# Kernel tuning notes

Hardware: AMD Instinct MI355X
Metric: run time of the kernel (lower is better)

The kernel has to match this reference:

```python
import jax, jax.numpy as jnp
import numpy as np

N = 2048      # num graph nodes (activities + places)
D = 256       # embedding_size
C = 3 * D     # cat_embedding_size
V = 2         # num variants
L = 16        # activities per variant
E = 16 * N    # edges for the encoder GNN
DEG_P = 0.0156  # adjacency density (~32 out-degree)


def setup_inputs() -> dict:
    key = jax.random.key(0)
    ks = jax.random.split(key, 6)
    embeddings = jax.random.normal(ks[0], (N, D), dtype=jnp.float32)
    W_self = jax.random.normal(ks[1], (D, D), dtype=jnp.float32) * 0.05
    W_nbr = jax.random.normal(ks[2], (D, D), dtype=jnp.float32) * 0.05
    b = jnp.zeros((D,), dtype=jnp.float32)
    variants = jax.random.randint(ks[3], (V, L), 0, N, dtype=jnp.int32)
    original = (jax.random.uniform(ks[4], (N, N)) < DEG_P).astype(jnp.int32)
    edge_index = jax.random.randint(ks[5], (2, E), 0, N, dtype=jnp.int32)
    return {"embeddings": embeddings, "W_self": W_self, "W_nbr": W_nbr, "b": b,
            "variants": variants, "original": original, "edge_index": edge_index}


def _forward(embeddings, W_self, W_nbr, b, variants, original, edge_index):
    n, d = embeddings.shape
    c = 3 * d
    dt = embeddings.dtype
    adj = original.astype(dt)              # [N,N]; adj[i,j]=1 iff edge i->j (forward star = row)
    src_e, dst_e = edge_index[0], edge_index[1]

    def encoder(x):
        # SecondEncoder approximated as one GCN-style message-passing layer
        msg = jax.ops.segment_sum(x[src_e], dst_e, num_segments=n)
        return jax.nn.relu(x @ W_self + msg @ W_nbr + b)

    def run_variant(acts):  # acts: [L] int32
        onehot = jax.nn.one_hot(acts, n, dtype=dt)                # [L,N]
        incl = jnp.flip(jnp.cumsum(jnp.flip(onehot, 0), 0), 0)    # sum_{j>=i} onehot[j]
        present_later = ((incl - onehot) > 0).astype(dt)          # set of nodes in acts[i+1:]

        def step(carry, inp):
            emb, pi, summary = carry
            a, plater = inp
            followers = adj[a]                                    # forward star of activity a
            has = jnp.any(followers > 0)
            adj_m = adj * plater[None, :]                         # edges into later-in-variant activities
            dest_cnt = adj_m.sum(axis=1)                          # |destination set| per candidate place
            dst_all = adj_m @ emb                                 # summed destination embeddings, [N,D]
            mask = jnp.where(has, ((followers > 0) & (dest_cnt > 0)).astype(dt), 0.0)
            # cat = (place_f, src_f, dst_f) per considered place
            cat = jnp.concatenate(
                [emb, jnp.broadcast_to(emb[a][None, :], emb.shape), dst_all], axis=1) * mask[:, None]
            pi = pi + cat                                         # places_info[place] += cat
            # prev_embedding_summary += places_info[place] for each considered place
            summary = summary + (mask[:, None] * pi).sum(axis=0)
            # places_info[considered] += prev_embedding_summary
            pi = pi + mask[:, None] * summary[None, :]
            emb = jnp.where(has, encoder(emb), emb)               # encoder skipped when no followers
            return (emb, pi, summary), None

        init = (embeddings, jnp.zeros((n, c), dt), jnp.zeros((c,), dt))
        (_, pi, _), _ = jax.lax.scan(step, init, (acts, present_later))
        return pi

    # variant shuffle in the original is irrelevant: embeddings reset each variant
    # and final_places_info is a sum over variants.
    return jax.vmap(run_variant)(variants).sum(axis=0)


def reference(embeddings, W_self, W_nbr, b, variants, original, edge_index):
    return _forward(embeddings, W_self, W_nbr, b, variants, original, edge_index)
```

## Files before the change

### kernel.cpp

```cpp
#include <hip/hip_runtime.h>

#define N 2048
#define D 256
#define C 768
#define V 2
#define L 16
#define NSTATE 15
#define NAPP 14
#define TCAP 256
#define FCAP 64

typedef __attribute__((ext_vector_type(8))) short bf16x8;
typedef __attribute__((ext_vector_type(4))) float f32x4;

__device__ __forceinline__ ushort bf16_rn(float x) {
  unsigned u = __float_as_uint(x);
  u += 0x7FFFu + ((u >> 16) & 1u);
  return (ushort)(u >> 16);
}
__device__ __forceinline__ float bf16_f(ushort h) {
  return __uint_as_float(((unsigned)h) << 16);
}

__device__ __forceinline__ size_t a_addr(int row, int k) {
  return ((size_t)(row >> 5) * 4 + (k >> 6)) * 2048 + (row & 31) * 64 + (k & 63);
}
__device__ __forceinline__ size_t wt_addr(int n, int k) {
  return ((size_t)(n >> 5) * 4 + (k >> 6)) * 2048 + (n & 31) * 64 + (k & 63);
}

__global__ __launch_bounds__(256) void k_init(
    const float* __restrict__ emb, const float* __restrict__ Ws,
    const float* __restrict__ Wn, float* __restrict__ states0,
    ushort* __restrict__ WtHi, ushort* __restrict__ WtLo,
    ushort* __restrict__ A0hi, ushort* __restrict__ A0lo,
    float* __restrict__ out,
    const int* __restrict__ adj, const int* __restrict__ variants,
    int* __restrict__ stepP, int* __restrict__ stepDm,
    int* __restrict__ stepCnt, int* __restrict__ hasG, int* __restrict__ tlG) {
  __shared__ int tl_sh[16];
  __shared__ int foll[FCAP], fbits[FCAP];
  __shared__ int sh_tc, sh_fcnt, sh_ecnt;
  int t = threadIdx.x;
  if (blockIdx.x < 512) {
    size_t i = (size_t)blockIdx.x * 256 + t;
    const size_t stride = (size_t)512 * 256;
    for (size_t x = i; x < (size_t)N * D; x += stride) {
      float v = emb[x];
      states0[x] = v;
      ushort h = bf16_rn(v);
      ushort l = bf16_rn(v - bf16_f(h));
      size_t a = a_addr((int)(x >> 8), (int)(x & 255));
      A0hi[a] = h;
      A0lo[a] = l;
    }
    for (size_t x = i; x < (size_t)512 * 256; x += stride) {
      int n = (int)(x >> 8), k = (int)(x & 255);
      float v = (n < 256) ? Ws[(size_t)k * 256 + n]
                          : Wn[(size_t)k * 256 + (n - 256)];
      ushort h = bf16_rn(v);
      size_t a = wt_addr(n, k);
      WtHi[a] = h;
      WtLo[a] = bf16_rn(v - bf16_f(h));
    }
    for (size_t x = i; x < (size_t)N * C; x += stride) out[x] = 0.f;
    return;
  }
  int vi = blockIdx.x - 512;
  int v = vi / L, i = vi % L;
  int a = variants[vi];
  if (t == 0) {
    int cnt = 0;
    for (int j = i + 1; j < L; j++) {
      int x = variants[v * L + j];
      bool dup = false;
      for (int q = 0; q < cnt; q++) if (tl_sh[q] == x) dup = true;
      if (!dup) tl_sh[cnt++] = x;
    }
    sh_tc = cnt;
    sh_fcnt = 0;
    sh_ecnt = 0;
    for (int q = 0; q < cnt; q++) tlG[vi * 16 + q] = tl_sh[q];
  }
  __syncthreads();
  for (int p = t; p < N; p += 256) {
    if (adj[(size_t)a * N + p] != 0) {
      int f = atomicAdd(&sh_fcnt, 1);
      if (f < FCAP) foll[f] = p;
    }
  }
  __syncthreads();
  int fc = sh_fcnt < FCAP ? sh_fcnt : FCAP;
  int tc = sh_tc;
  for (int x = t; x < fc; x += 256) fbits[x] = 0;
  __syncthreads();
  for (int x = t; x < fc * tc; x += 256) {
    int fi = x / tc, q = x - fi * tc;
    if (adj[(size_t)foll[fi] * N + tl_sh[q]] != 0) atomicOr(&fbits[fi], 1 << q);
  }
  __syncthreads();
  for (int fi = t; fi < fc; fi += 256) {
    int bits = fbits[fi];
    if (bits) {
      int e = atomicAdd(&sh_ecnt, 1);
      stepP[vi * FCAP + e] = foll[fi];
      stepDm[vi * FCAP + e] = bits;
    }
  }
  __syncthreads();
  if (t == 0) {
    stepCnt[vi] = sh_ecnt;
    hasG[vi] = (sh_fcnt > 0);
  }
}

__global__ __launch_bounds__(1024) void k_scan(const int* __restrict__ ei,
                                               int E, int* __restrict__ fillpos,
                                               int* __restrict__ row_ptr) {
  __shared__ int hist[N];
  __shared__ int part[256];
  __shared__ int base[257];
  int t = threadIdx.x;
  for (int p = t; p < N; p += 1024) hist[p] = 0;
  __syncthreads();
  const int e4 = E >> 2;
  const int4* dsts = (const int4*)(ei + E);
  for (int g = t; g < e4; g += 1024) {
    int4 d = dsts[g];
    atomicAdd(&hist[d.x], 1);
    atomicAdd(&hist[d.y], 1);
    atomicAdd(&hist[d.z], 1);
    atomicAdd(&hist[d.w], 1);
  }
  for (int e = (e4 << 2) + t; e < E; e += 1024) atomicAdd(&hist[ei[E + e]], 1);
  __syncthreads();
  int v[8];
  int s = 0;
  if (t < 256) {
    for (int j = 0; j < 8; j++) { v[j] = hist[t * 8 + j]; s += v[j]; }
  }
  __syncthreads();
  if (t < 256) part[t] = s;
  __syncthreads();
  if (t == 0) {
    int acc = 0;
    for (int q = 0; q < 256; q++) { base[q] = acc; acc += part[q]; }
    base[256] = acc;
  }
  __syncthreads();
  if (t < 256) {
    int acc = base[t];
    for (int j = 0; j < 8; j++) {
      row_ptr[t * 8 + j] = acc;
      fillpos[t * 8 + j] = acc;
      acc += v[j];
    }
    if (t == 255) row_ptr[N] = base[256];
  }
}

__global__ __launch_bounds__(256) void k_fillB(
    const int* __restrict__ ei, int E, int* __restrict__ fillpos,
    int* __restrict__ csr_src,
    const int* __restrict__ stepP, const int* __restrict__ stepDm,
    const int* __restrict__ stepCnt, const int* __restrict__ hasG,
    int* __restrict__ entP, int* __restrict__ entPrev, int* __restrict__ entDm,
    int* __restrict__ offsG, int* __restrict__ kidxG, int* __restrict__ cmatG,
    int* __restrict__ lastPG, int* __restrict__ lastIG, int* __restrict__ lastMG,
    int* __restrict__ cntG) {
  __shared__ int pmask[N];
  __shared__ int sP[16][FCAP];
  __shared__ int sDm[16][FCAP];
  __shared__ int cnt[16], offs[17];
  __shared__ int cmat_sh[256];
  __shared__ int sh_u;
  int t = threadIdx.x;
  if (blockIdx.x < 128) {
    for (int e = blockIdx.x * 256 + t; e < E; e += 128 * 256) {
      int dst = ei[E + e];
      int pos = atomicAdd(&fillpos[dst], 1);
      csr_src[pos] = ei[e];
    }
    return;
  }
  int v = blockIdx.x - 128;
  for (int p = t; p < N; p += 256) pmask[p] = 0;
  for (int x = t; x < 256; x += 256) cmat_sh[x] = 0;
  if (t < 16) cnt[t] = stepCnt[v * L + t];
  if (t == 0) sh_u = 0;
  __syncthreads();
  if (t == 0) {
    int acc = 0;
    for (int i = 0; i < 16; i++) {
      offs[i] = acc < TCAP ? acc : TCAP;
      acc += cnt[i];
    }
    offs[16] = acc < TCAP ? acc : TCAP;
    cntG[v * 2 + 0] = offs[16];
    int k = 0;
    for (int i = 0; i < L; i++) {
      kidxG[v * 16 + i] = k;
      if (hasG[v * L + i]) k++;
    }
  }
  for (int x = t; x < 16 * FCAP; x += 256) {
    int i = x >> 6, f = x & 63;
    if (f < stepCnt[v * L + i]) {
      int p = stepP[(v * L + i) * FCAP + f];
      sP[i][f] = p;
      sDm[i][f] = stepDm[(v * L + i) * FCAP + f];
      atomicOr(&pmask[p], 1 << i);
    }
  }
  __syncthreads();
  for (int x = t; x < 16 * FCAP; x += 256) {
    int i = x >> 6, f = x & 63;
    if (f < cnt[i]) {
      int e = offs[i] + f;
      if (e < TCAP) {
        int p = sP[i][f];
        entP[v * TCAP + e] = p;
        entDm[v * TCAP + e] = sDm[i][f];
        int m = pmask[p] & ((1 << i) - 1);
        int prev = -1;
        if (m) {
          int j = 31 - __clz(m);
          int cj = cnt[j];
          for (int f2 = 0; f2 < cj; f2++)
            if (sP[j][f2] == p) { prev = offs[j] + f2; break; }
        }
        entPrev[v * TCAP + e] = prev;
      }
    }
  }
  __syncthreads();
  for (int p = t; p < N; p += 256) {
    int m = pmask[p];
    if (m) {
      int u = atomicAdd(&sh_u, 1);
      int j = 31 - __clz(m);
      int li = -1;
      int cj = cnt[j];
      for (int f2 = 0; f2 < cj; f2++)
        if (sP[j][f2] == p) { li = offs[j] + f2; break; }
      lastPG[v * TCAP + u] = p;
      lastIG[v * TCAP + u] = li;
      lastMG[v * TCAP + u] = m;
      int mm = m;
      while (mm) {
        int bi = __ffs(mm) - 1; mm &= mm - 1;
        int m2 = m & ((1 << bi) - 1);
        while (m2) {
          int bj = __ffs(m2) - 1; m2 &= m2 - 1;
          atomicAdd(&cmat_sh[bi * 16 + bj], 1);
        }
      }
    }
  }
  __syncthreads();
  if (t == 0) cntG[v * 2 + 1] = sh_u;
  for (int x = t; x < 256; x += 256) cmatG[v * 256 + x] = cmat_sh[x];
  for (int x = t; x < 17; x += 256) offsG[v * 17 + x] = offs[x];
}

__global__ __launch_bounds__(256) void k_gemm(
    const ushort* __restrict__ Ah, const ushort* __restrict__ Al,
    const ushort* __restrict__ Wh_g, const ushort* __restrict__ Wl_g,
    float* __restrict__ Z) {
  __shared__ __align__(16) ushort Ash[2][32][72], Asl[2][32][72];
  __shared__ __align__(16) ushort Wsh[2][32][72], Wsl[2][32][72];
  const int tid = threadIdx.x, wave = tid >> 6, lane = tid & 63;
  const int quad = lane >> 4, l16 = lane & 15;
  const int wr = wave >> 1, wc = wave & 1;
  const int mb = blockIdx.x, nb = blockIdx.y;
  const int sr = tid >> 3, sc = (tid & 7) * 8;

  f32x4 acc = {0.f, 0.f, 0.f, 0.f};
  size_t abase = (size_t)mb * 4 * 2048 + (size_t)tid * 8;
  size_t wbase = (size_t)nb * 4 * 2048 + (size_t)tid * 8;
  {
    uint4 ra  = *(const uint4*)&Ah[abase];
    uint4 rl  = *(const uint4*)&Al[abase];
    uint4 rwh = *(const uint4*)&Wh_g[wbase];
    uint4 rwl = *(const uint4*)&Wl_g[wbase];
    *(uint4*)&Ash[0][sr][sc] = ra;
    *(uint4*)&Asl[0][sr][sc] = rl;
    *(uint4*)&Wsh[0][sr][sc] = rwh;
    *(uint4*)&Wsl[0][sr][sc] = rwl;
  }
  __syncthreads();
#pragma unroll
  for (int c = 0; c < 4; c++) {
    const int rb = c & 1;
    uint4 ra, rl, rwh, rwl;
    if (c < 3) {
      size_t o = (size_t)(c + 1) * 2048;
      ra  = *(const uint4*)&Ah[abase + o];
      rl  = *(const uint4*)&Al[abase + o];
      rwh = *(const uint4*)&Wh_g[wbase + o];
      rwl = *(const uint4*)&Wl_g[wbase + o];
    }
#pragma unroll
    for (int kf = 0; kf < 2; kf++) {
      int ko = kf * 32 + quad * 8;
      bf16x8 a_h = *(const bf16x8*)&Ash[rb][wr * 16 + l16][ko];
      bf16x8 a_l = *(const bf16x8*)&Asl[rb][wr * 16 + l16][ko];
      bf16x8 w_h = *(const bf16x8*)&Wsh[rb][wc * 16 + l16][ko];
      bf16x8 w_l = *(const bf16x8*)&Wsl[rb][wc * 16 + l16][ko];
      acc = __builtin_amdgcn_mfma_f32_16x16x32_bf16(a_h, w_h, acc, 0, 0, 0);
      acc = __builtin_amdgcn_mfma_f32_16x16x32_bf16(a_h, w_l, acc, 0, 0, 0);
      acc = __builtin_amdgcn_mfma_f32_16x16x32_bf16(a_l, w_h, acc, 0, 0, 0);
    }
    if (c < 3) {
      const int wb = rb ^ 1;
      *(uint4*)&Ash[wb][sr][sc] = ra;
      *(uint4*)&Asl[wb][sr][sc] = rl;
      *(uint4*)&Wsh[wb][sr][sc] = rwh;
      *(uint4*)&Wsl[wb][sr][sc] = rwl;
      __syncthreads();
    }
  }
  int col = nb * 32 + wc * 16 + l16;
  int row0 = mb * 32 + wr * 16 + quad * 4;
#pragma unroll
  for (int r = 0; r < 4; r++)
    Z[(size_t)(row0 + r) * 512 + col] = acc[r];
}

__global__ __launch_bounds__(256) void k_comb(
    const float* __restrict__ Z, const float* __restrict__ bias,
    const int* __restrict__ row_ptr, const int* __restrict__ csr_src,
    float* __restrict__ stnext, ushort* __restrict__ NAh,
    ushort* __restrict__ NAl) {
  int row = blockIdx.x * 4 + (threadIdx.x >> 6);
  int lane = threadIdx.x & 63;
  const float4* Zp = (const float4*)Z;
  float4 acc = Zp[(size_t)row * 128 + lane];
  float4 acc2 = {0.f, 0.f, 0.f, 0.f};
  float4 acc3 = {0.f, 0.f, 0.f, 0.f};
  float4 acc4 = {0.f, 0.f, 0.f, 0.f};
  int e0 = row_ptr[row], e1 = row_ptr[row + 1];
  int e = e0;
  for (; e + 3 < e1; e += 4) {
    int s0 = csr_src[e], s1 = csr_src[e + 1];
    int s2 = csr_src[e + 2], s3 = csr_src[e + 3];
    float4 x0 = Zp[(size_t)s0 * 128 + 64 + lane];
    float4 x1 = Zp[(size_t)s1 * 128 + 64 + lane];
    float4 x2 = Zp[(size_t)s2 * 128 + 64 + lane];
    float4 x3 = Zp[(size_t)s3 * 128 + 64 + lane];
    acc.x += x0.x; acc.y += x0.y; acc.z += x0.z; acc.w += x0.w;
    acc2.x += x1.x; acc2.y += x1.y; acc2.z += x1.z; acc2.w += x1.w;
    acc3.x += x2.x; acc3.y += x2.y; acc3.z += x2.z; acc3.w += x2.w;
    acc4.x += x3.x; acc4.y += x3.y; acc4.z += x3.z; acc4.w += x3.w;
  }
  for (; e < e1; e++) {
    float4 x0 = Zp[(size_t)csr_src[e] * 128 + 64 + lane];
    acc.x += x0.x; acc.y += x0.y; acc.z += x0.z; acc.w += x0.w;
  }
  float4 bv = ((const float4*)bias)[lane];
  float v0 = fmaxf(acc.x + acc2.x + acc3.x + acc4.x + bv.x, 0.f);
  float v1 = fmaxf(acc.y + acc2.y + acc3.y + acc4.y + bv.y, 0.f);
  float v2 = fmaxf(acc.z + acc2.z + acc3.z + acc4.z + bv.z, 0.f);
  float v3 = fmaxf(acc.w + acc2.w + acc3.w + acc4.w + bv.w, 0.f);
  *(float4*)(stnext + (size_t)row * D + lane * 4) = make_float4(v0, v1, v2, v3);
  ushort h0 = bf16_rn(v0), h1 = bf16_rn(v1), h2 = bf16_rn(v2), h3 = bf16_rn(v3);
  size_t ca = a_addr(row, lane * 4);
  *(ushort4*)&NAh[ca] = make_ushort4(h0, h1, h2, h3);
  *(ushort4*)&NAl[ca] = make_ushort4(
      bf16_rn(v0 - bf16_f(h0)), bf16_rn(v1 - bf16_f(h1)),
      bf16_rn(v2 - bf16_f(h2)), bf16_rn(v3 - bf16_f(h3)));
}

#define PI_LDS_BYTES (TCAP * 64 * 4 + 16 * 64 * 4 + 16 * 64 * 4 + 256 * 4 + \
                      3 * TCAP * 4 + 17 * 4 + 16 * 4 + 256 * 4)
__global__ __launch_bounds__(512) void k_pi(
    const float* __restrict__ states, float* __restrict__ out,
    const int* __restrict__ variants,
    const int* __restrict__ entP, const int* __restrict__ entPrev,
    const int* __restrict__ entDm, const int* __restrict__ offsG,
    const int* __restrict__ kidxG, const int* __restrict__ tlG,
    const int* __restrict__ cmatG, const int* __restrict__ lastPG,
    const int* __restrict__ lastIG, const int* __restrict__ lastMG,
    const int* __restrict__ cntG) {
  extern __shared__ __align__(16) float smf[];
  float* catb = smf;
  float* S_lds = catb + TCAP * 64;
  float* aS = S_lds + 16 * 64;
  float* cmatf = aS + 16 * 64;
  int* eP  = (int*)(cmatf + 256);
  int* ePr = eP + TCAP;
  int* eDm = ePr + TCAP;
  int* offs = eDm + TCAP;
  int* kidx = offs + 17;
  int* tl = kidx + 16;
  int v = blockIdx.x / 12, cgi = blockIdx.x % 12;
  int grp = cgi >> 2;
  int tid = threadIdx.x, lane = tid & 63, w = tid >> 6;
  int cl = (cgi & 3) * 64 + lane;
  int col = cgi * 64 + lane;

  int T = cntG[v * 2 + 0], U = cntG[v * 2 + 1];
  for (int x = tid; x < T; x += 512) {
    eP[x] = entP[v * TCAP + x];
    ePr[x] = entPrev[v * TCAP + x];
    eDm[x] = entDm[v * TCAP + x];
  }
  for (int x = tid; x < 17; x += 512) offs[x] = offsG[v * 17 + x];
  if (tid < 16) kidx[tid] = kidxG[v * 16 + tid];
  for (int x = tid; x < 256; x += 512) {
    tl[x] = tlG[v * 256 + x];
    cmatf[x] = (float)cmatG[v * 256 + x];
  }
  __syncthreads();

  for (int i = 0; i < L; i++) {
    int kk = kidx[i]; if (kk > NSTATE - 1) kk = NSTATE - 1;
    const float* embS = states + (size_t)kk * N * D;
    int o0 = offs[i], o1 = offs[i + 1];
    if (grp == 0) {
      for (int e = o0 + w; e < o1; e += 8)
        catb[e * 64 + lane] = embS[(size_t)eP[e] * D + cl];
    } else if (grp == 1) {
      float embA = embS[(size_t)variants[v * L + i] * D + cl];
      for (int e = o0 + w; e < o1; e += 8) catb[e * 64 + lane] = embA;
    } else {
      for (int e = o0 + w; e < o1; e += 8) {
        float sa = 0.f;
        int bm = eDm[e];
        while (bm) {
          int q = __ffs(bm) - 1; bm &= bm - 1;
          sa += embS[(size_t)tl[i * 16 + q] * D + cl];
        }
        catb[e * 64 + lane] = sa;
      }
    }
  }
  __syncthreads();
  for (int u = w; u < U; u += 8) {
    int li = lastIG[v * TCAP + u];
    int len = 0;
    for (int c2 = li; c2 >= 0; c2 = ePr[c2]) len++;
    for (int j = 1; j < len; j++) {
      int c2 = li;
      for (int k = 0; k < len - 1 - j; k++) c2 = ePr[c2];
      catb[c2 * 64 + lane] += catb[ePr[c2] * 64 + lane];
    }
  }
  __syncthreads();
  for (int i = w; i < 16; i += 8) {
    float a = 0.f;
    for (int e = offs[i]; e < offs[i + 1]; e++) a += catb[e * 64 + lane];
    aS[i * 64 + lane] = a;
  }
  __syncthreads();
  if (w == 0) {
    float S[16];
    float Sp = 0.f;
#pragma unroll
    for (int i = 0; i < 16; i++) {
      float sv = Sp + aS[i * 64 + lane];
#pragma unroll
      for (int j = 0; j < 16; j++)
        if (j < i) sv += cmatf[i * 16 + j] * S[j];
      S[i] = sv;
      S_lds[i * 64 + lane] = sv;
      Sp = sv;
    }
  }
  __syncthreads();
  for (int u = w; u < U; u += 8) {
    int p = lastPG[v * TCAP + u];
    int li = lastIG[v * TCAP + u];
    int m = lastMG[v * TCAP + u];
    float acc = catb[li * 64 + lane];
    while (m) {
      int q = __ffs(m) - 1; m &= m - 1;
      acc += S_lds[q * 64 + lane];
    }
    atomicAdd(&out[(size_t)p * C + col], acc);
  }
}

extern "C" void kernel_launch(void* const* d_in, const int* in_sizes, int n_in,
                              void* d_out, int out_size, void* d_ws, size_t ws_size,
                              hipStream_t stream) {
  const float* emb      = (const float*)d_in[0];
  const float* Ws       = (const float*)d_in[1];
  const float* Wn       = (const float*)d_in[2];
  const float* bias     = (const float*)d_in[3];
  const int*   variants = (const int*)d_in[4];
  const int*   adj      = (const int*)d_in[5];
  const int*   ei       = (const int*)d_in[6];
  const int    E        = in_sizes[6] / 2;
  float* out            = (float*)d_out;

  char* base = (char*)d_ws;
  float* states = (float*)base;            base += (size_t)NSTATE * N * D * 4;
  float* Z      = (float*)base;            base += (size_t)N * 512 * 4;
  ushort* WtHi  = (ushort*)base;           base += (size_t)512 * 256 * 2;
  ushort* WtLo  = (ushort*)base;           base += (size_t)512 * 256 * 2;
  ushort* A0h   = (ushort*)base;           base += (size_t)N * D * 2;
  ushort* A0l   = (ushort*)base;           base += (size_t)N * D * 2;
  ushort* A1h   = (ushort*)base;           base += (size_t)N * D * 2;
  ushort* A1l   = (ushort*)base;           base += (size_t)N * D * 2;
  int* row_ptr  = (int*)base;              base += (N + 1) * 4;
  int* fillpos  = (int*)base;              base += N * 4;
  int* csr_src  = (int*)base;              base += (size_t)E * 4;
  int* stepP    = (int*)base;              base += V * L * FCAP * 4;
  int* stepDm   = (int*)base;              base += V * L * FCAP * 4;
  int* stepCnt  = (int*)base;              base += V * L * 4;
  int* hasG     = (int*)base;              base += V * L * 4;
  int* entP     = (int*)base;              base += V * TCAP * 4;
  int* entPrev  = (int*)base;              base += V * TCAP * 4;
  int* entDm    = (int*)base;              base += V * TCAP * 4;
  int* offsG    = (int*)base;              base += V * 17 * 4;
  int* kidxG    = (int*)base;              base += V * 16 * 4;
  int* tlG      = (int*)base;              base += V * 256 * 4;
  int* cmatG    = (int*)base;              base += V * 256 * 4;
  int* lastPG   = (int*)base;              base += V * TCAP * 4;
  int* lastIG   = (int*)base;              base += V * TCAP * 4;
  int* lastMG   = (int*)base;              base += V * TCAP * 4;
  int* cntG     = (int*)base;              base += V * 2 * 4;

  hipFuncSetAttribute((const void*)k_pi,
                      hipFuncAttributeMaxDynamicSharedMemorySize, PI_LDS_BYTES);

  k_init<<<512 + V * L, 256, 0, stream>>>(emb, Ws, Wn, states, WtHi, WtLo,
                                          A0h, A0l, out, adj, variants,
                                          stepP, stepDm, stepCnt, hasG, tlG);
  k_scan<<<1, 1024, 0, stream>>>(ei, E, fillpos, row_ptr);
  k_fillB<<<128 + V, 256, 0, stream>>>(ei, E, fillpos, csr_src, stepP, stepDm,
                                       stepCnt, hasG, entP, entPrev, entDm,
                                       offsG, kidxG, cmatG, lastPG, lastIG,
                                       lastMG, cntG);

  ushort* AH[2] = {A0h, A1h};
  ushort* AL[2] = {A0l, A1l};
  for (int s = 0; s < NAPP; s++) {
    int cur = s & 1, nxt = cur ^ 1;
    k_gemm<<<dim3(64, 16), 256, 0, stream>>>(AH[cur], AL[cur], WtHi, WtLo, Z);
    k_comb<<<N / 4, 256, 0, stream>>>(Z, bias, row_ptr, csr_src,
                                      states + (size_t)(s + 1) * N * D,
                                      AH[nxt], AL[nxt]);
  }
  k_pi<<<V * 12, 512, PI_LDS_BYTES, stream>>>(states, out, variants, entP,
                                              entPrev, entDm, offsG, kidxG, tlG,
                                              cmatG, lastPG, lastIG, lastMG,
                                              cntG);
}
```

Measured before the change: 339.4 us.

## Fold CSR scan and fill setup kernels into init and first GEMM launches

The single-block histogram/scan kernel becomes an extra block of k_init. The CSR fill and per-variant bookkeeping blocks move into extra grid rows of a first GEMM launch that shares its LDS buffer. This removes two serial kernel launches and lets the setup work overlap with init and the first GEMM. The neighbour gather in k_comb is also unrolled to 8 accumulators for more memory-level parallelism. The scan block now runs with 256 threads instead of 1024, so the histogram loop is slower, but it runs beside the other init blocks.

After: 334.5 us. No clear change (-1.4%).

```diff
diff --git a/kernel.cpp b/kernel.cpp
--- a/kernel.cpp
+++ b/kernel.cpp
@@ -37,10 +37,15 @@
     float* __restrict__ out,
     const int* __restrict__ adj, const int* __restrict__ variants,
     int* __restrict__ stepP, int* __restrict__ stepDm,
-    int* __restrict__ stepCnt, int* __restrict__ hasG, int* __restrict__ tlG) {
+    int* __restrict__ stepCnt, int* __restrict__ hasG, int* __restrict__ tlG,
+    const int* __restrict__ ei, int E, int* __restrict__ fillpos,
+    int* __restrict__ row_ptr) {
   __shared__ int tl_sh[16];
   __shared__ int foll[FCAP], fbits[FCAP];
   __shared__ int sh_tc, sh_fcnt, sh_ecnt;
+  __shared__ int hist[N];
+  __shared__ int part[256];
+  __shared__ int base[257];
   int t = threadIdx.x;
   if (blockIdx.x < 512) {
     size_t i = (size_t)blockIdx.x * 256 + t;
@@ -66,81 +71,74 @@
     for (size_t x = i; x < (size_t)N * C; x += stride) out[x] = 0.f;
     return;
   }
-  int vi = blockIdx.x - 512;
-  int v = vi / L, i = vi % L;
-  int a = variants[vi];
-  if (t == 0) {
-    int cnt = 0;
-    for (int j = i + 1; j < L; j++) {
-      int x = variants[v * L + j];
-      bool dup = false;
-      for (int q = 0; q < cnt; q++) if (tl_sh[q] == x) dup = true;
-      if (!dup) tl_sh[cnt++] = x;
-    }
-    sh_tc = cnt;
-    sh_fcnt = 0;
-    sh_ecnt = 0;
-    for (int q = 0; q < cnt; q++) tlG[vi * 16 + q] = tl_sh[q];
-  }
-  __syncthreads();
-  for (int p = t; p < N; p += 256) {
-    if (adj[(size_t)a * N + p] != 0) {
-      int f = atomicAdd(&sh_fcnt, 1);
-      if (f < FCAP) foll[f] = p;
-    }
-  }
-  __syncthreads();
-  int fc = sh_fcnt < FCAP ? sh_fcnt : FCAP;
-  int tc = sh_tc;
-  for (int x = t; x < fc; x += 256) fbits[x] = 0;
-  __syncthreads();
-  for (int x = t; x < fc * tc; x += 256) {
-    int fi = x / tc, q = x - fi * tc;
-    if (adj[(size_t)foll[fi] * N + tl_sh[q]] != 0) atomicOr(&fbits[fi], 1 << q);
-  }
-  __syncthreads();
-  for (int fi = t; fi < fc; fi += 256) {
-    int bits = fbits[fi];
-    if (bits) {
-      int e = atomicAdd(&sh_ecnt, 1);
-      stepP[vi * FCAP + e] = foll[fi];
-      stepDm[vi * FCAP + e] = bits;
-    }
-  }
-  __syncthreads();
-  if (t == 0) {
-    stepCnt[vi] = sh_ecnt;
-    hasG[vi] = (sh_fcnt > 0);
-  }
-}
-
-__global__ __launch_bounds__(1024) void k_scan(const int* __restrict__ ei,
-                                               int E, int* __restrict__ fillpos,
-                                               int* __restrict__ row_ptr) {
-  __shared__ int hist[N];
-  __shared__ int part[256];
-  __shared__ int base[257];
-  int t = threadIdx.x;
-  for (int p = t; p < N; p += 1024) hist[p] = 0;
-  __syncthreads();
-  const int e4 = E >> 2;
-  const int4* dsts = (const int4*)(ei + E);
-  for (int g = t; g < e4; g += 1024) {
-    int4 d = dsts[g];
-    atomicAdd(&hist[d.x], 1);
-    atomicAdd(&hist[d.y], 1);
-    atomicAdd(&hist[d.z], 1);
-    atomicAdd(&hist[d.w], 1);
-  }
-  for (int e = (e4 << 2) + t; e < E; e += 1024) atomicAdd(&hist[ei[E + e]], 1);
-  __syncthreads();
-  int v[8];
+  if (blockIdx.x < 544) {
+    int vi = blockIdx.x - 512;
+    int v = vi / L, i = vi % L;
+    int a = variants[vi];
+    if (t == 0) {
+      int cnt = 0;
+      for (int j = i + 1; j < L; j++) {
+        int x = variants[v * L + j];
+        bool dup = false;
+        for (int q = 0; q < cnt; q++) if (tl_sh[q] == x) dup = true;
+        if (!dup) tl_sh[cnt++] = x;
+      }
+      sh_tc = cnt;
+      sh_fcnt = 0;
+      sh_ecnt = 0;
+      for (int q = 0; q < cnt; q++) tlG[vi * 16 + q] = tl_sh[q];
+    }
+    __syncthreads();
+    for (int p = t; p < N; p += 256) {
+      if (adj[(size_t)a * N + p] != 0) {
+        int f = atomicAdd(&sh_fcnt, 1);
+        if (f < FCAP) foll[f] = p;
+      }
+    }
+    __syncthreads();
+    int fc = sh_fcnt < FCAP ? sh_fcnt : FCAP;
+    int tc = sh_tc;
+    for (int x = t; x < fc; x += 256) fbits[x] = 0;
+    __syncthreads();
+    for (int x = t; x < fc * tc; x += 256) {
+      int fi = x / tc, q = x - fi * tc;
+      if (adj[(size_t)foll[fi] * N + tl_sh[q]] != 0) atomicOr(&fbits[fi], 1 << q);
+    }
+    __syncthreads();
+    for (int fi = t; fi < fc; fi += 256) {
+      int bits = fbits[fi];
+      if (bits) {
+        int e = atomicAdd(&sh_ecnt, 1);
+        stepP[vi * FCAP + e] = foll[fi];
+        stepDm[vi * FCAP + e] = bits;
+      }
+    }
+    __syncthreads();
+    if (t == 0) {
+      stepCnt[vi] = sh_ecnt;
+      hasG[vi] = (sh_fcnt > 0);
+    }
+    return;
+  }
+  for (int p = t; p < N; p += 256) hist[p] = 0;
+  __syncthreads();
+  {
+    const int e4 = E >> 2;
+    const int4* dsts = (const int4*)(ei + E);
+    for (int g = t; g < e4; g += 256) {
+      int4 d = dsts[g];
+      atomicAdd(&hist[d.x], 1);
+      atomicAdd(&hist[d.y], 1);
+      atomicAdd(&hist[d.z], 1);
+      atomicAdd(&hist[d.w], 1);
+    }
+    for (int e = (e4 << 2) + t; e < E; e += 256) atomicAdd(&hist[ei[E + e]], 1);
+  }
+  __syncthreads();
+  int vv[8];
   int s = 0;
-  if (t < 256) {
-    for (int j = 0; j < 8; j++) { v[j] = hist[t * 8 + j]; s += v[j]; }
-  }
-  __syncthreads();
-  if (t < 256) part[t] = s;
+  for (int j = 0; j < 8; j++) { vv[j] = hist[t * 8 + j]; s += vv[j]; }
+  part[t] = s;
   __syncthreads();
   if (t == 0) {
     int acc = 0;
@@ -148,131 +146,27 @@
     base[256] = acc;
   }
   __syncthreads();
-  if (t < 256) {
-    int acc = base[t];
-    for (int j = 0; j < 8; j++) {
-      row_ptr[t * 8 + j] = acc;
-      fillpos[t * 8 + j] = acc;
-      acc += v[j];
-    }
-    if (t == 255) row_ptr[N] = base[256];
-  }
-}
-
-__global__ __launch_bounds__(256) void k_fillB(
-    const int* __restrict__ ei, int E, int* __restrict__ fillpos,
-    int* __restrict__ csr_src,
-    const int* __restrict__ stepP, const int* __restrict__ stepDm,
-    const int* __restrict__ stepCnt, const int* __restrict__ hasG,
-    int* __restrict__ entP, int* __restrict__ entPrev, int* __restrict__ entDm,
-    int* __restrict__ offsG, int* __restrict__ kidxG, int* __restrict__ cmatG,
-    int* __restrict__ lastPG, int* __restrict__ lastIG, int* __restrict__ lastMG,
-    int* __restrict__ cntG) {
-  __shared__ int pmask[N];
-  __shared__ int sP[16][FCAP];
-  __shared__ int sDm[16][FCAP];
-  __shared__ int cnt[16], offs[17];
-  __shared__ int cmat_sh[256];
-  __shared__ int sh_u;
-  int t = threadIdx.x;
-  if (blockIdx.x < 128) {
-    for (int e = blockIdx.x * 256 + t; e < E; e += 128 * 256) {
-      int dst = ei[E + e];
-      int pos = atomicAdd(&fillpos[dst], 1);
-      csr_src[pos] = ei[e];
-    }
-    return;
-  }
-  int v = blockIdx.x - 128;
-  for (int p = t; p < N; p += 256) pmask[p] = 0;
-  for (int x = t; x < 256; x += 256) cmat_sh[x] = 0;
-  if (t < 16) cnt[t] = stepCnt[v * L + t];
-  if (t == 0) sh_u = 0;
-  __syncthreads();
-  if (t == 0) {
-    int acc = 0;
-    for (int i = 0; i < 16; i++) {
-      offs[i] = acc < TCAP ? acc : TCAP;
-      acc += cnt[i];
-    }
-    offs[16] = acc < TCAP ? acc : TCAP;
-    cntG[v * 2 + 0] = offs[16];
-    int k = 0;
-    for (int i = 0; i < L; i++) {
-      kidxG[v * 16 + i] = k;
-      if (hasG[v * L + i]) k++;
-    }
-  }
-  for (int x = t; x < 16 * FCAP; x += 256) {
-    int i = x >> 6, f = x & 63;
-    if (f < stepCnt[v * L + i]) {
-      int p = stepP[(v * L + i) * FCAP + f];
-      sP[i][f] = p;
-      sDm[i][f] = stepDm[(v * L + i) * FCAP + f];
-      atomicOr(&pmask[p], 1 << i);
-    }
-  }
-  __syncthreads();
-  for (int x = t; x < 16 * FCAP; x += 256) {
-    int i = x >> 6, f = x & 63;
-    if (f < cnt[i]) {
-      int e = offs[i] + f;
-      if (e < TCAP) {
-        int p = sP[i][f];
-        entP[v * TCAP + e] = p;
-        entDm[v * TCAP + e] = sDm[i][f];
-        int m = pmask[p] & ((1 << i) - 1);
-        int prev = -1;
-        if (m) {
-          int j = 31 - __clz(m);
-          int cj = cnt[j];
-          for (int f2 = 0; f2 < cj; f2++)
-            if (sP[j][f2] == p) { prev = offs[j] + f2; break; }
-        }
-        entPrev[v * TCAP + e] = prev;
-      }
-    }
-  }
-  __syncthreads();
-  for (int p = t; p < N; p += 256) {
-    int m = pmask[p];
-    if (m) {
-      int u = atomicAdd(&sh_u, 1);
-      int j = 31 - __clz(m);
-      int li = -1;
-      int cj = cnt[j];
-      for (int f2 = 0; f2 < cj; f2++)
-        if (sP[j][f2] == p) { li = offs[j] + f2; break; }
-      lastPG[v * TCAP + u] = p;
-      lastIG[v * TCAP + u] = li;
-      lastMG[v * TCAP + u] = m;
-      int mm = m;
-      while (mm) {
-        int bi = __ffs(mm) - 1; mm &= mm - 1;
-        int m2 = m & ((1 << bi) - 1);
-        while (m2) {
-          int bj = __ffs(m2) - 1; m2 &= m2 - 1;
-          atomicAdd(&cmat_sh[bi * 16 + bj], 1);
-        }
-      }
-    }
-  }
-  __syncthreads();
-  if (t == 0) cntG[v * 2 + 1] = sh_u;
-  for (int x = t; x < 256; x += 256) cmatG[v * 256 + x] = cmat_sh[x];
-  for (int x = t; x < 17; x += 256) offsG[v * 17 + x] = offs[x];
-}
-
-__global__ __launch_bounds__(256) void k_gemm(
+  int acc = base[t];
+  for (int j = 0; j < 8; j++) {
+    row_ptr[t * 8 + j] = acc;
+    fillpos[t * 8 + j] = acc;
+    acc += vv[j];
+  }
+  if (t == 255) row_ptr[N] = base[256];
+}
+
+__device__ __forceinline__ void gemm_body(
     const ushort* __restrict__ Ah, const ushort* __restrict__ Al,
     const ushort* __restrict__ Wh_g, const ushort* __restrict__ Wl_g,
-    float* __restrict__ Z) {
-  __shared__ __align__(16) ushort Ash[2][32][72], Asl[2][32][72];
-  __shared__ __align__(16) ushort Wsh[2][32][72], Wsl[2][32][72];
-  const int tid = threadIdx.x, wave = tid >> 6, lane = tid & 63;
+    float* __restrict__ Z, ushort* smem, const int mb, const int nb,
+    const int tid) {
+  ushort (*Ash)[32][72] = (ushort (*)[32][72])(smem);
+  ushort (*Asl)[32][72] = (ushort (*)[32][72])(smem + 4608);
+  ushort (*Wsh)[32][72] = (ushort (*)[32][72])(smem + 9216);
+  ushort (*Wsl)[32][72] = (ushort (*)[32][72])(smem + 13824);
+  const int wave = tid >> 6, lane = tid & 63;
   const int quad = lane >> 4, l16 = lane & 15;
   const int wr = wave >> 1, wc = wave & 1;
-  const int mb = blockIdx.x, nb = blockIdx.y;
   const int sr = tid >> 3, sc = (tid & 7) * 8;
 
   f32x4 acc = {0.f, 0.f, 0.f, 0.f};
@@ -327,6 +221,129 @@
     Z[(size_t)(row0 + r) * 512 + col] = acc[r];
 }
 
+__global__ __launch_bounds__(256) void k_gemm(
+    const ushort* __restrict__ Ah, const ushort* __restrict__ Al,
+    const ushort* __restrict__ Wh_g, const ushort* __restrict__ Wl_g,
+    float* __restrict__ Z) {
+  __shared__ __align__(16) ushort smem[18432];
+  gemm_body(Ah, Al, Wh_g, Wl_g, Z, smem, blockIdx.x, blockIdx.y, threadIdx.x);
+}
+
+__global__ __launch_bounds__(256) void k_gemm0(
+    const ushort* __restrict__ Ah, const ushort* __restrict__ Al,
+    const ushort* __restrict__ Wh_g, const ushort* __restrict__ Wl_g,
+    float* __restrict__ Z,
+    const int* __restrict__ ei, int E, int* __restrict__ fillpos,
+    int* __restrict__ csr_src,
+    const int* __restrict__ stepP, const int* __restrict__ stepDm,
+    const int* __restrict__ stepCnt, const int* __restrict__ hasG,
+    int* __restrict__ entP, int* __restrict__ entPrev, int* __restrict__ entDm,
+    int* __restrict__ offsG, int* __restrict__ kidxG, int* __restrict__ cmatG,
+    int* __restrict__ lastPG, int* __restrict__ lastIG, int* __restrict__ lastMG,
+    int* __restrict__ cntG) {
+  __shared__ __align__(16) ushort smem[18432];
+  int t = threadIdx.x;
+  if (blockIdx.y < 16) {
+    gemm_body(Ah, Al, Wh_g, Wl_g, Z, smem, blockIdx.x, blockIdx.y, t);
+    return;
+  }
+  int aux = (blockIdx.y - 16) * 64 + blockIdx.x;
+  if (aux < 128) {
+    for (int e = aux * 256 + t; e < E; e += 128 * 256) {
+      int dst = ei[E + e];
+      int pos = atomicAdd(&fillpos[dst], 1);
+      csr_src[pos] = ei[e];
+    }
+    return;
+  }
+  if (aux >= 128 + V) return;
+  int vb = aux - 128;
+  int* pmask = (int*)smem;
+  int (*sP)[FCAP] = (int (*)[FCAP])(pmask + N);
+  int (*sDm)[FCAP] = (int (*)[FCAP])((int*)sP + 16 * FCAP);
+  int* cnt = (int*)sDm + 16 * FCAP;
+  int* offs = cnt + 16;
+  int* cmat_sh = offs + 17;
+  int* sh_u = cmat_sh + 256;
+  for (int p = t; p < N; p += 256) pmask[p] = 0;
+  for (int x = t; x < 256; x += 256) cmat_sh[x] = 0;
+  if (t < 16) cnt[t] = stepCnt[vb * L + t];
+  if (t == 0) *sh_u = 0;
+  __syncthreads();
+  if (t == 0) {
+    int acc = 0;
+    for (int i = 0; i < 16; i++) {
+      offs[i] = acc < TCAP ? acc : TCAP;
+      acc += cnt[i];
+    }
+    offs[16] = acc < TCAP ? acc : TCAP;
+    cntG[vb * 2 + 0] = offs[16];
+    int k = 0;
+    for (int i = 0; i < L; i++) {
+      kidxG[vb * 16 + i] = k;
+      if (hasG[vb * L + i]) k++;
+    }
+  }
+  for (int x = t; x < 16 * FCAP; x += 256) {
+    int i = x >> 6, f = x & 63;
+    if (f < stepCnt[vb * L + i]) {
+      int p = stepP[(vb * L + i) * FCAP + f];
+      sP[i][f] = p;
+      sDm[i][f] = stepDm[(vb * L + i) * FCAP + f];
+      atomicOr(&pmask[p], 1 << i);
+    }
+  }
+  __syncthreads();
+  for (int x = t; x < 16 * FCAP; x += 256) {
+    int i = x >> 6, f = x & 63;
+    if (f < cnt[i]) {
+      int e = offs[i] + f;
+      if (e < TCAP) {
+        int p = sP[i][f];
+        entP[vb * TCAP + e] = p;
+        entDm[vb * TCAP + e] = sDm[i][f];
+        int m = pmask[p] & ((1 << i) - 1);
+        int prev = -1;
+        if (m) {
+          int j = 31 - __clz(m);
+          int cj = cnt[j];
+          for (int f2 = 0; f2 < cj; f2++)
+            if (sP[j][f2] == p) { prev = offs[j] + f2; break; }
+        }
+        entPrev[vb * TCAP + e] = prev;
+      }
+    }
+  }
+  __syncthreads();
+  for (int p = t; p < N; p += 256) {
+    int m = pmask[p];
+    if (m) {
+      int u = atomicAdd(sh_u, 1);
+      int j = 31 - __clz(m);
+      int li = -1;
+      int cj = cnt[j];
+      for (int f2 = 0; f2 < cj; f2++)
+        if (sP[j][f2] == p) { li = offs[j] + f2; break; }
+      lastPG[vb * TCAP + u] = p;
+      lastIG[vb * TCAP + u] = li;
+      lastMG[vb * TCAP + u] = m;
+      int mm = m;
+      while (mm) {
+        int bi = __ffs(mm) - 1; mm &= mm - 1;
+        int m2 = m & ((1 << bi) - 1);
+        while (m2) {
+          int bj = __ffs(m2) - 1; m2 &= m2 - 1;
+          atomicAdd(&cmat_sh[bi * 16 + bj], 1);
+        }
+      }
+    }
+  }
+  __syncthreads();
+  if (t == 0) cntG[vb * 2 + 1] = *sh_u;
+  for (int x = t; x < 256; x += 256) cmatG[vb * 256 + x] = cmat_sh[x];
+  for (int x = t; x < 17; x += 256) offsG[vb * 17 + x] = offs[x];
+}
+
 __global__ __launch_bounds__(256) void k_comb(
     const float* __restrict__ Z, const float* __restrict__ bias,
     const int* __restrict__ row_ptr, const int* __restrict__ csr_src,
@@ -335,33 +352,59 @@
   int row = blockIdx.x * 4 + (threadIdx.x >> 6);
   int lane = threadIdx.x & 63;
   const float4* Zp = (const float4*)Z;
-  float4 acc = Zp[(size_t)row * 128 + lane];
-  float4 acc2 = {0.f, 0.f, 0.f, 0.f};
-  float4 acc3 = {0.f, 0.f, 0.f, 0.f};
-  float4 acc4 = {0.f, 0.f, 0.f, 0.f};
+  float4 self = Zp[(size_t)row * 128 + lane];
+  float4 b0 = {0.f, 0.f, 0.f, 0.f}, b1 = b0, b2 = b0, b3 = b0;
+  float4 b4 = b0, b5 = b0, b6 = b0, b7 = b0;
   int e0 = row_ptr[row], e1 = row_ptr[row + 1];
   int e = e0;
-  for (; e + 3 < e1; e += 4) {
-    int s0 = csr_src[e], s1 = csr_src[e + 1];
+  for (; e + 7 < e1; e += 8) {
+    int s0 = csr_src[e],     s1 = csr_src[e + 1];
+    int s2 = csr_src[e + 2], s3 = csr_src[e + 3];
+    int s4 = csr_src[e + 4], s5 = csr_src[e + 5];
+    int s6 = csr_src[e + 6], s7 = csr_src[e + 7];
+    float4 x0 = Zp[(size_t)s0 * 128 + 64 + lane];
+    float4 x1 = Zp[(size_t)s1 * 128 + 64 + lane];
+    float4 x2 = Zp[(size_t)s2 * 128 + 64 + lane];
+    float4 x3 = Zp[(size_t)s3 * 128 + 64 + lane];
+    float4 x4 = Zp[(size_t)s4 * 128 + 64 + lane];
+    float4 x5 = Zp[(size_t)s5 * 128 + 64 + lane];
+    float4 x6 = Zp[(size_t)s6 * 128 + 64 + lane];
+    float4 x7 = Zp[(size_t)s7 * 128 + 64 + lane];
+    b0.x += x0.x; b0.y += x0.y; b0.z += x0.z; b0.w += x0.w;
+    b1.x += x1.x; b1.y += x1.y; b1.z += x1.z; b1.w += x1.w;
+    b2.x += x2.x; b2.y += x2.y; b2.z += x2.z; b2.w += x2.w;
+    b3.x += x3.x; b3.y += x3.y; b3.z += x3.z; b3.w += x3.w;
+    b4.x += x4.x; b4.y += x4.y; b4.z += x4.z; b4.w += x4.w;
+    b5.x += x5.x; b5.y += x5.y; b5.z += x5.z; b5.w += x5.w;
+    b6.x += x6.x; b6.y += x6.y; b6.z += x6.z; b6.w += x6.w;
+    b7.x += x7.x; b7.y += x7.y; b7.z += x7.z; b7.w += x7.w;
+  }
+  if (e + 3 < e1) {
+    int s0 = csr_src[e],     s1 = csr_src[e + 1];
     int s2 = csr_src[e + 2], s3 = csr_src[e + 3];
     float4 x0 = Zp[(size_t)s0 * 128 + 64 + lane];
     float4 x1 = Zp[(size_t)s1 * 128 + 64 + lane];
     float4 x2 = Zp[(size_t)s2 * 128 + 64 + lane];
     float4 x3 = Zp[(size_t)s3 * 128 + 64 + lane];
-    acc.x += x0.x; acc.y += x0.y; acc.z += x0.z; acc.w += x0.w;
-    acc2.x += x1.x; acc2.y += x1.y; acc2.z += x1.z; acc2.w += x1.w;
-    acc3.x += x2.x; acc3.y += x2.y; acc3.z += x2.z; acc3.w += x2.w;
-    acc4.x += x3.x; acc4.y += x3.y; acc4.z += x3.z; acc4.w += x3.w;
+    b0.x += x0.x; b0.y += x0.y; b0.z += x0.z; b0.w += x0.w;
+    b1.x += x1.x; b1.y += x1.y; b1.z += x1.z; b1.w += x1.w;
+    b2.x += x2.x; b2.y += x2.y; b2.z += x2.z; b2.w += x2.w;
+    b3.x += x3.x; b3.y += x3.y; b3.z += x3.z; b3.w += x3.w;
+    e += 4;
   }
   for (; e < e1; e++) {
     float4 x0 = Zp[(size_t)csr_src[e] * 128 + 64 + lane];
-    acc.x += x0.x; acc.y += x0.y; acc.z += x0.z; acc.w += x0.w;
+    b0.x += x0.x; b0.y += x0.y; b0.z += x0.z; b0.w += x0.w;
   }
   float4 bv = ((const float4*)bias)[lane];
-  float v0 = fmaxf(acc.x + acc2.x + acc3.x + acc4.x + bv.x, 0.f);
-  float v1 = fmaxf(acc.y + acc2.y + acc3.y + acc4.y + bv.y, 0.f);
-  float v2 = fmaxf(acc.z + acc2.z + acc3.z + acc4.z + bv.z, 0.f);
-  float v3 = fmaxf(acc.w + acc2.w + acc3.w + acc4.w + bv.w, 0.f);
+  float v0 = fmaxf(self.x + ((b0.x + b1.x) + (b2.x + b3.x)) +
+                   ((b4.x + b5.x) + (b6.x + b7.x)) + bv.x, 0.f);
+  float v1 = fmaxf(self.y + ((b0.y + b1.y) + (b2.y + b3.y)) +
+                   ((b4.y + b5.y) + (b6.y + b7.y)) + bv.y, 0.f);
+  float v2 = fmaxf(self.z + ((b0.z + b1.z) + (b2.z + b3.z)) +
+                   ((b4.z + b5.z) + (b6.z + b7.z)) + bv.z, 0.f);
+  float v3 = fmaxf(self.w + ((b0.w + b1.w) + (b2.w + b3.w)) +
+                   ((b4.w + b5.w) + (b6.w + b7.w)) + bv.w, 0.f);
   *(float4*)(stnext + (size_t)row * D + lane * 4) = make_float4(v0, v1, v2, v3);
   ushort h0 = bf16_rn(v0), h1 = bf16_rn(v1), h2 = bf16_rn(v2), h3 = bf16_rn(v3);
   size_t ca = a_addr(row, lane * 4);
@@ -525,18 +568,19 @@
   hipFuncSetAttribute((const void*)k_pi,
                       hipFuncAttributeMaxDynamicSharedMemorySize, PI_LDS_BYTES);
 
-  k_init<<<512 + V * L, 256, 0, stream>>>(emb, Ws, Wn, states, WtHi, WtLo,
-                                          A0h, A0l, out, adj, variants,
-                                          stepP, stepDm, stepCnt, hasG, tlG);
-  k_scan<<<1, 1024, 0, stream>>>(ei, E, fillpos, row_ptr);
-  k_fillB<<<128 + V, 256, 0, stream>>>(ei, E, fillpos, csr_src, stepP, stepDm,
-                                       stepCnt, hasG, entP, entPrev, entDm,
-                                       offsG, kidxG, cmatG, lastPG, lastIG,
-                                       lastMG, cntG);
+  k_init<<<545, 256, 0, stream>>>(emb, Ws, Wn, states, WtHi, WtLo, A0h, A0l,
+                                  out, adj, variants, stepP, stepDm, stepCnt,
+                                  hasG, tlG, ei, E, fillpos, row_ptr);
+  k_gemm0<<<dim3(64, 19), 256, 0, stream>>>(
+      A0h, A0l, WtHi, WtLo, Z, ei, E, fillpos, csr_src, stepP, stepDm,
+      stepCnt, hasG, entP, entPrev, entDm, offsG, kidxG, cmatG, lastPG,
+      lastIG, lastMG, cntG);
+  k_comb<<<N / 4, 256, 0, stream>>>(Z, bias, row_ptr, csr_src,
+                                    states + (size_t)1 * N * D, A1h, A1l);
 
   ushort* AH[2] = {A0h, A1h};
   ushort* AL[2] = {A0l, A1l};
-  for (int s = 0; s < NAPP; s++) {
+  for (int s = 1; s < NAPP; s++) {
     int cur = s & 1, nxt = cur ^ 1;
     k_gemm<<<dim3(64, 16), 256, 0, stream>>>(AH[cur], AL[cur], WtHi, WtLo, Z);
     k_comb<<<N / 4, 256, 0, stream>>>(Z, bias, row_ptr, csr_src,
```
